# Performance work log

Measured on AMD Instinct MI355X. Metric: run time of the kernel, lower is better.

Reference implementation:

```python
import jax, jax.numpy as jnp
import numpy as np
import math

EPS = 1e-8


def _l2_normalize(v, axis=-1, eps=EPS):
    # Matches torch.nn.functional.normalize: v / max(||v||, eps)
    n = jnp.sqrt(jnp.sum(v * v, axis=axis, keepdims=True))
    return v / jnp.maximum(n, eps)


def _gelu_tanh(x):
    c = math.sqrt(2.0 / math.pi)
    return 0.5 * x * (1.0 + jnp.tanh(c * (x + 0.044715 * x * x * x)))


def setup_inputs() -> dict:
    key = jax.random.key(0)
    k1, k2, k3, k4 = jax.random.split(key, 4)
    B, T, D, K = 8, 4096, 2048, 8
    x = jax.random.normal(k1, (B, T, D), dtype=jnp.float32)
    # module initializes prototypes as normalized randn(K, D)
    P = jax.random.normal(k2, (K, D), dtype=jnp.float32)
    P = _l2_normalize(P)
    log_tau = jnp.asarray(math.log(2.0), dtype=jnp.float32)
    log_blend = jnp.asarray(math.log(0.3 / 0.7), dtype=jnp.float32)
    return {"x": x, "prototypes": P, "log_tau": log_tau, "log_blend": log_blend}


def reference(x, prototypes, log_tau, log_blend):
    tau = jnp.exp(log_tau)
    alpha = jax.nn.sigmoid(log_blend)
    B, T, D = x.shape
    x_norm = _l2_normalize(x)                      # (B, T, D)
    p_norm = _l2_normalize(prototypes)             # (K, D)
    sims = jnp.einsum('btd,kd->btk', x_norm, p_norm)  # tiny K=8 matmul
    sims = jnp.clip(sims, -1.0, 1.0)
    min_dist = jnp.min(1.0 - sims, axis=-1)        # (B, T)
    min_dist = jnp.clip(min_dist, 0.0, 2.0)
    novelty = 1.0 - jnp.exp(-tau * min_dist)       # (B, T)
    scale = 1.0 - alpha + alpha * novelty[..., None]
    scale = jnp.clip(scale, 0.1, 10.0)
    return _gelu_tanh(x * scale)
```

## Files before the change

kernel.cpp:

```cpp
#include <hip/hip_runtime.h>
#include <math.h>

#define D 2048
#define K 8
#define BLOCK 256
#define ROWS 2
#define CHUNK 16

typedef __fp16 h2 __attribute__((ext_vector_type(2)));

__device__ __forceinline__ float rcp_fast(float x) {
    return __builtin_amdgcn_rcpf(x);
}

#if __has_builtin(__builtin_amdgcn_fdot2)
#define FDOT2(a, b, c) __builtin_amdgcn_fdot2((a), (b), (c), false)
#else
__device__ __forceinline__ float fdot2_emul(h2 a, h2 b, float c) {
    return fmaf((float)a[0], (float)b[0], fmaf((float)a[1], (float)b[1], c));
}
#define FDOT2 fdot2_emul
#endif

__device__ __forceinline__ float gelu_tanh_fast(float y) {
    const float nc = -2.3022078977f;
    float w = y * fmaf(0.044715f, y * y, 1.0f);
    return y * rcp_fast(1.0f + exp2f(nc * w));
}

__device__ __forceinline__ float dot4(const float4& a, const float4& b) {
    return fmaf(a.w, b.w, fmaf(a.z, b.z, fmaf(a.y, b.y, a.x * b.x)));
}

#define FOLDSTEP(x, y, m)                                   \
    {                                                       \
        float _k = (lane & (m)) ? (y) : (x);                \
        float _o = (lane & (m)) ? (x) : (y);                \
        x = _k + __shfl_xor(_o, (m));                       \
    }

__global__ __launch_bounds__(BLOCK, 4)
void novelty_gelu_kernel(const float* __restrict__ x,
                         const float* __restrict__ P,
                         const float* __restrict__ plog_tau,
                         const float* __restrict__ plog_blend,
                         float* __restrict__ out,
                         int nrows)
{
    __shared__ float s_inv[K];
    __shared__ float redT[2][ROWS][12][4];

    const int tid  = threadIdx.x;
    const int wave = tid >> 6;
    const int lane = tid & 63;
    const int col  = tid * 8;

    for (int k = wave; k < K; k += 4) {
        const float* pr = P + k * D;
        float s = 0.f;
        #pragma unroll
        for (int j = 0; j < 8; ++j) {
            float4 p = *(const float4*)(pr + j * 256 + lane * 4);
            s += dot4(p, p);
        }
        #pragma unroll
        for (int m = 1; m < 64; m <<= 1) s += __shfl_xor(s, m);
        if (lane == 0) s_inv[k] = 1.0f / fmaxf(sqrtf(s), 1e-8f);
    }
    __syncthreads();

    h2 pf[K][4];
    #pragma unroll
    for (int k = 0; k < K; ++k) {
        const float inv = s_inv[k];
        float4 p0 = *(const float4*)(P + k * D + col);
        float4 p1 = *(const float4*)(P + k * D + col + 4);
        pf[k][0] = __builtin_amdgcn_cvt_pkrtz(p0.x * inv, p0.y * inv);
        pf[k][1] = __builtin_amdgcn_cvt_pkrtz(p0.z * inv, p0.w * inv);
        pf[k][2] = __builtin_amdgcn_cvt_pkrtz(p1.x * inv, p1.y * inv);
        pf[k][3] = __builtin_amdgcn_cvt_pkrtz(p1.z * inv, p1.w * inv);
    }

    const float tau   = __expf(plog_tau[0]);
    const float alpha = 1.0f / (1.0f + __expf(-plog_blend[0]));
    const float oma   = 1.0f - alpha;

    const int base  = blockIdx.x * CHUNK;
    const int limit = base + CHUNK;
    int row = base;
    int buf = 0;

    float4 a[ROWS][2], b[ROWS][2];
    {
        #pragma unroll
        for (int r = 0; r < ROWS; ++r) {
            const float* xr = x + (size_t)(row + r) * D + col;
            a[r][0] = *(const float4*)(xr);
            a[r][1] = *(const float4*)(xr + 4);
        }
    }

    while (row < limit) {
        const int nr = row + ROWS;
        if (nr < limit) {
            #pragma unroll
            for (int r = 0; r < ROWS; ++r) {
                const float* xn = x + (size_t)(nr + r) * D + col;
                b[r][0] = *(const float4*)(xn);
                b[r][1] = *(const float4*)(xn + 4);
            }
        }

        #pragma unroll
        for (int r = 0; r < ROWS; ++r) {
            h2 xh[4];
            xh[0] = __builtin_amdgcn_cvt_pkrtz(a[r][0].x, a[r][0].y);
            xh[1] = __builtin_amdgcn_cvt_pkrtz(a[r][0].z, a[r][0].w);
            xh[2] = __builtin_amdgcn_cvt_pkrtz(a[r][1].x, a[r][1].y);
            xh[3] = __builtin_amdgcn_cvt_pkrtz(a[r][1].z, a[r][1].w);

            float ssq = 0.f;
            float dt[K];
            #pragma unroll
            for (int k = 0; k < K; ++k) dt[k] = 0.f;
            #pragma unroll
            for (int i = 0; i < 4; ++i) {
                ssq = FDOT2(xh[i], xh[i], ssq);
                #pragma unroll
                for (int k = 0; k < K; ++k)
                    dt[k] = FDOT2(xh[i], pf[k][i], dt[k]);
            }

            FOLDSTEP(dt[0], dt[1], 1);
            FOLDSTEP(dt[2], dt[3], 1);
            FOLDSTEP(dt[4], dt[5], 1);
            FOLDSTEP(dt[6], dt[7], 1);
            FOLDSTEP(dt[0], dt[2], 2);
            FOLDSTEP(dt[4], dt[6], 2);
            FOLDSTEP(dt[0], dt[4], 4);
            float vd = dt[0];
            vd += __shfl_xor(vd, 8);
            vd += __shfl_xor(vd, 16);
            vd += __shfl_xor(vd, 32);

            #pragma unroll
            for (int m = 1; m < 64; m <<= 1) ssq += __shfl_xor(ssq, m);

            if (lane < 8)       redT[buf][r][lane][wave] = vd;
            else if (lane == 8) redT[buf][r][8][wave]    = ssq;
        }

        __syncthreads();

        #pragma unroll
        for (int r = 0; r < ROWS; ++r) {
            float4 qs = *(const float4*)&redT[buf][r][8][0];
            float tssq = (qs.x + qs.y) + (qs.z + qs.w);
            float dmax = -3.0e38f;
            #pragma unroll
            for (int k = 0; k < K; ++k) {
                float4 q = *(const float4*)&redT[buf][r][k][0];
                dmax = fmaxf(dmax, (q.x + q.y) + (q.z + q.w));
            }
            const float inv_nx = 1.0f / fmaxf(sqrtf(tssq), 1e-8f);
            float sim = fminf(1.0f, fmaxf(-1.0f, dmax * inv_nx));
            float md  = fminf(fmaxf(1.0f - sim, 0.0f), 2.0f);
            float scale = oma + alpha * (1.0f - __expf(-tau * md));
            scale = fminf(fmaxf(scale, 0.1f), 10.0f);

            float* outr = out + (size_t)(row + r) * D + col;
            float4 o0, o1;
            o0.x = gelu_tanh_fast(a[r][0].x * scale);
            o0.y = gelu_tanh_fast(a[r][0].y * scale);
            o0.z = gelu_tanh_fast(a[r][0].z * scale);
            o0.w = gelu_tanh_fast(a[r][0].w * scale);
            o1.x = gelu_tanh_fast(a[r][1].x * scale);
            o1.y = gelu_tanh_fast(a[r][1].y * scale);
            o1.z = gelu_tanh_fast(a[r][1].z * scale);
            o1.w = gelu_tanh_fast(a[r][1].w * scale);
            *(float4*)(outr)     = o0;
            *(float4*)(outr + 4) = o1;
        }

        #pragma unroll
        for (int r = 0; r < ROWS; ++r) { a[r][0] = b[r][0]; a[r][1] = b[r][1]; }
        row = nr;
        buf ^= 1;
    }
}

extern "C" void kernel_launch(void* const* d_in, const int* in_sizes, int n_in,
                              void* d_out, int out_size, void* d_ws, size_t ws_size,
                              hipStream_t stream) {
    const float* x  = (const float*)d_in[0];
    const float* P  = (const float*)d_in[1];
    const float* lt = (const float*)d_in[2];
    const float* lb = (const float*)d_in[3];
    float* out = (float*)d_out;

    const int nrows = in_sizes[0] / D;
    int grid = nrows / CHUNK;

    novelty_gelu_kernel<<<grid, BLOCK, 0, stream>>>(x, P, lt, lb, out, nrows);
}
```

Before: 123.2 us.

## Assign one wave per row and keep normalized prototypes in LDS

Changes the work split so each 64-lane wave reduces a full 2048-wide row with shuffles only. This removes the cross-wave shared-memory reduction and the per-row-pair block barrier. The fp16-packed normalized prototypes move from per-thread registers into a shared LDS table read each iteration. The block grows to 512 threads with 4 rows per wave. The GELU output is now computed from the fp16-rounded copy of x, which lowers register pressure but reduces output precision. The explicit next-row prefetch is dropped in favor of more concurrent waves.

New measurement: 331.9 us. +169.5%, slower.

```diff
diff --git a/kernel.cpp b/kernel.cpp
--- a/kernel.cpp
+++ b/kernel.cpp
@@ -3,11 +3,11 @@
 
 #define D 2048
 #define K 8
-#define BLOCK 256
-#define ROWS 2
-#define CHUNK 16
+#define BLOCK 512
+#define RPW 4
 
 typedef __fp16 h2 __attribute__((ext_vector_type(2)));
+typedef __fp16 h4 __attribute__((ext_vector_type(4)));
 
 __device__ __forceinline__ float rcp_fast(float x) {
     return __builtin_amdgcn_rcpf(x);
@@ -28,7 +28,7 @@
     return y * rcp_fast(1.0f + exp2f(nc * w));
 }
 
-__device__ __forceinline__ float dot4(const float4& a, const float4& b) {
+__device__ __forceinline__ float dot4f(const float4& a, const float4& b) {
     return fmaf(a.w, b.w, fmaf(a.z, b.z, fmaf(a.y, b.y, a.x * b.x)));
 }
 
@@ -39,153 +39,121 @@
         x = _k + __shfl_xor(_o, (m));                       \
     }
 
-__global__ __launch_bounds__(BLOCK, 4)
-void novelty_gelu_kernel(const float* __restrict__ x,
-                         const float* __restrict__ P,
-                         const float* __restrict__ plog_tau,
-                         const float* __restrict__ plog_blend,
-                         float* __restrict__ out,
-                         int nrows)
+__global__ __launch_bounds__(BLOCK, 8)
+void novelty_gelu_wave(const float* __restrict__ x,
+                       const float* __restrict__ P,
+                       const float* __restrict__ plog_tau,
+                       const float* __restrict__ plog_blend,
+                       float* __restrict__ out,
+                       int nrows)
 {
+    __shared__ h4    pf[K * 512];
     __shared__ float s_inv[K];
-    __shared__ float redT[2][ROWS][12][4];
 
     const int tid  = threadIdx.x;
     const int wave = tid >> 6;
     const int lane = tid & 63;
-    const int col  = tid * 8;
 
-    for (int k = wave; k < K; k += 4) {
-        const float* pr = P + k * D;
+    {
+        const float* pr = P + wave * D;
         float s = 0.f;
         #pragma unroll
         for (int j = 0; j < 8; ++j) {
-            float4 p = *(const float4*)(pr + j * 256 + lane * 4);
-            s += dot4(p, p);
+            float4 p = *(const float4*)(pr + (j * 64 + lane) * 4);
+            s += dot4f(p, p);
         }
         #pragma unroll
         for (int m = 1; m < 64; m <<= 1) s += __shfl_xor(s, m);
-        if (lane == 0) s_inv[k] = 1.0f / fmaxf(sqrtf(s), 1e-8f);
+        if (lane == 0) s_inv[wave] = 1.0f / fmaxf(sqrtf(s), 1e-8f);
     }
     __syncthreads();
 
-    h2 pf[K][4];
     #pragma unroll
     for (int k = 0; k < K; ++k) {
         const float inv = s_inv[k];
-        float4 p0 = *(const float4*)(P + k * D + col);
-        float4 p1 = *(const float4*)(P + k * D + col + 4);
-        pf[k][0] = __builtin_amdgcn_cvt_pkrtz(p0.x * inv, p0.y * inv);
-        pf[k][1] = __builtin_amdgcn_cvt_pkrtz(p0.z * inv, p0.w * inv);
-        pf[k][2] = __builtin_amdgcn_cvt_pkrtz(p1.x * inv, p1.y * inv);
-        pf[k][3] = __builtin_amdgcn_cvt_pkrtz(p1.z * inv, p1.w * inv);
+        float4 p = *(const float4*)(P + k * D + tid * 4);
+        h2 lo = __builtin_amdgcn_cvt_pkrtz(p.x * inv, p.y * inv);
+        h2 hi = __builtin_amdgcn_cvt_pkrtz(p.z * inv, p.w * inv);
+        pf[k * 512 + tid] = __builtin_shufflevector(lo, hi, 0, 1, 2, 3);
     }
+    __syncthreads();
 
     const float tau   = __expf(plog_tau[0]);
     const float alpha = 1.0f / (1.0f + __expf(-plog_blend[0]));
     const float oma   = 1.0f - alpha;
 
-    const int base  = blockIdx.x * CHUNK;
-    const int limit = base + CHUNK;
-    int row = base;
-    int buf = 0;
+    const int wid = blockIdx.x * (BLOCK / 64) + wave;
+    int row = wid * RPW;
+    int limit = row + RPW;
+    if (limit > nrows) limit = nrows;
 
-    float4 a[ROWS][2], b[ROWS][2];
-    {
+    for (; row < limit; ++row) {
+        const float* xr = x + (size_t)row * D;
+
+        float4 v[8];
         #pragma unroll
-        for (int r = 0; r < ROWS; ++r) {
-            const float* xr = x + (size_t)(row + r) * D + col;
-            a[r][0] = *(const float4*)(xr);
-            a[r][1] = *(const float4*)(xr + 4);
+        for (int c = 0; c < 8; ++c)
+            v[c] = *(const float4*)(xr + (c * 64 + lane) * 4);
+
+        h2 xh[16];
+        #pragma unroll
+        for (int c = 0; c < 8; ++c) {
+            xh[2 * c]     = __builtin_amdgcn_cvt_pkrtz(v[c].x, v[c].y);
+            xh[2 * c + 1] = __builtin_amdgcn_cvt_pkrtz(v[c].z, v[c].w);
         }
-    }
 
-    while (row < limit) {
-        const int nr = row + ROWS;
-        if (nr < limit) {
+        float ssq = 0.f;
+        float dt[K];
+        #pragma unroll
+        for (int k = 0; k < K; ++k) dt[k] = 0.f;
+        #pragma unroll
+        for (int c = 0; c < 8; ++c) {
+            ssq = FDOT2(xh[2 * c],     xh[2 * c],     ssq);
+            ssq = FDOT2(xh[2 * c + 1], xh[2 * c + 1], ssq);
             #pragma unroll
-            for (int r = 0; r < ROWS; ++r) {
-                const float* xn = x + (size_t)(nr + r) * D + col;
-                b[r][0] = *(const float4*)(xn);
-                b[r][1] = *(const float4*)(xn + 4);
+            for (int k = 0; k < K; ++k) {
+                h4 p  = pf[k * 512 + c * 64 + lane];
+                h2 lo = __builtin_shufflevector(p, p, 0, 1);
+                h2 hi = __builtin_shufflevector(p, p, 2, 3);
+                dt[k] = FDOT2(xh[2 * c],     lo, dt[k]);
+                dt[k] = FDOT2(xh[2 * c + 1], hi, dt[k]);
             }
         }
 
+        FOLDSTEP(dt[0], dt[1], 1);
+        FOLDSTEP(dt[2], dt[3], 1);
+        FOLDSTEP(dt[4], dt[5], 1);
+        FOLDSTEP(dt[6], dt[7], 1);
+        FOLDSTEP(dt[0], dt[2], 2);
+        FOLDSTEP(dt[4], dt[6], 2);
+        FOLDSTEP(dt[0], dt[4], 4);
+        float vd = dt[0];
+        vd += __shfl_xor(vd, 8);
+        vd += __shfl_xor(vd, 16);
+        vd += __shfl_xor(vd, 32);
+        float dmax = vd;
+        dmax = fmaxf(dmax, __shfl_xor(dmax, 1));
+        dmax = fmaxf(dmax, __shfl_xor(dmax, 2));
+        dmax = fmaxf(dmax, __shfl_xor(dmax, 4));
         #pragma unroll
-        for (int r = 0; r < ROWS; ++r) {
-            h2 xh[4];
-            xh[0] = __builtin_amdgcn_cvt_pkrtz(a[r][0].x, a[r][0].y);
-            xh[1] = __builtin_amdgcn_cvt_pkrtz(a[r][0].z, a[r][0].w);
-            xh[2] = __builtin_amdgcn_cvt_pkrtz(a[r][1].x, a[r][1].y);
-            xh[3] = __builtin_amdgcn_cvt_pkrtz(a[r][1].z, a[r][1].w);
+        for (int m = 1; m < 64; m <<= 1) ssq += __shfl_xor(ssq, m);
 
-            float ssq = 0.f;
-            float dt[K];
-            #pragma unroll
-            for (int k = 0; k < K; ++k) dt[k] = 0.f;
-            #pragma unroll
-            for (int i = 0; i < 4; ++i) {
-                ssq = FDOT2(xh[i], xh[i], ssq);
-                #pragma unroll
-                for (int k = 0; k < K; ++k)
-                    dt[k] = FDOT2(xh[i], pf[k][i], dt[k]);
-            }
+        const float inv_nx = 1.0f / fmaxf(sqrtf(ssq), 1e-8f);
+        float sim = fminf(1.0f, fmaxf(-1.0f, dmax * inv_nx));
+        float md  = fminf(fmaxf(1.0f - sim, 0.0f), 2.0f);
+        float scale = oma + alpha * (1.0f - __expf(-tau * md));
+        scale = fminf(fmaxf(scale, 0.1f), 10.0f);
 
-            FOLDSTEP(dt[0], dt[1], 1);
-            FOLDSTEP(dt[2], dt[3], 1);
-            FOLDSTEP(dt[4], dt[5], 1);
-            FOLDSTEP(dt[6], dt[7], 1);
-            FOLDSTEP(dt[0], dt[2], 2);
-            FOLDSTEP(dt[4], dt[6], 2);
-            FOLDSTEP(dt[0], dt[4], 4);
-            float vd = dt[0];
-            vd += __shfl_xor(vd, 8);
-            vd += __shfl_xor(vd, 16);
-            vd += __shfl_xor(vd, 32);
-
-            #pragma unroll
-            for (int m = 1; m < 64; m <<= 1) ssq += __shfl_xor(ssq, m);
-
-            if (lane < 8)       redT[buf][r][lane][wave] = vd;
-            else if (lane == 8) redT[buf][r][8][wave]    = ssq;
+        float* outr = out + (size_t)row * D;
+        #pragma unroll
+        for (int c = 0; c < 8; ++c) {
+            float4 o;
+            o.x = gelu_tanh_fast((float)xh[2 * c][0]     * scale);
+            o.y = gelu_tanh_fast((float)xh[2 * c][1]     * scale);
+            o.z = gelu_tanh_fast((float)xh[2 * c + 1][0] * scale);
+            o.w = gelu_tanh_fast((float)xh[2 * c + 1][1] * scale);
+            *(float4*)(outr + (c * 64 + lane) * 4) = o;
         }
-
-        __syncthreads();
-
-        #pragma unroll
-        for (int r = 0; r < ROWS; ++r) {
-            float4 qs = *(const float4*)&redT[buf][r][8][0];
-            float tssq = (qs.x + qs.y) + (qs.z + qs.w);
-            float dmax = -3.0e38f;
-            #pragma unroll
-            for (int k = 0; k < K; ++k) {
-                float4 q = *(const float4*)&redT[buf][r][k][0];
-                dmax = fmaxf(dmax, (q.x + q.y) + (q.z + q.w));
-            }
-            const float inv_nx = 1.0f / fmaxf(sqrtf(tssq), 1e-8f);
-            float sim = fminf(1.0f, fmaxf(-1.0f, dmax * inv_nx));
-            float md  = fminf(fmaxf(1.0f - sim, 0.0f), 2.0f);
-            float scale = oma + alpha * (1.0f - __expf(-tau * md));
-            scale = fminf(fmaxf(scale, 0.1f), 10.0f);
-
-            float* outr = out + (size_t)(row + r) * D + col;
-            float4 o0, o1;
-            o0.x = gelu_tanh_fast(a[r][0].x * scale);
-            o0.y = gelu_tanh_fast(a[r][0].y * scale);
-            o0.z = gelu_tanh_fast(a[r][0].z * scale);
-            o0.w = gelu_tanh_fast(a[r][0].w * scale);
-            o1.x = gelu_tanh_fast(a[r][1].x * scale);
-            o1.y = gelu_tanh_fast(a[r][1].y * scale);
-            o1.z = gelu_tanh_fast(a[r][1].z * scale);
-            o1.w = gelu_tanh_fast(a[r][1].w * scale);
-            *(float4*)(outr)     = o0;
-            *(float4*)(outr + 4) = o1;
-        }
-
-        #pragma unroll
-        for (int r = 0; r < ROWS; ++r) { a[r][0] = b[r][0]; a[r][1] = b[r][1]; }
-        row = nr;
-        buf ^= 1;
     }
 }
 
@@ -199,7 +167,8 @@
     float* out = (float*)d_out;
 
     const int nrows = in_sizes[0] / D;
-    int grid = nrows / CHUNK;
+    const int waves = BLOCK / 64;
+    int grid = (nrows + waves * RPW - 1) / (waves * RPW);
 
-    novelty_gelu_kernel<<<grid, BLOCK, 0, stream>>>(x, P, lt, lb, out, nrows);
+    novelty_gelu_wave<<<grid, BLOCK, 0, stream>>>(x, P, lt, lb, out, nrows);
 }
```
